# Optimization experiments

Measured on AMD Instinct MI355X. Metric: run time of the kernel, lower is better.

The kernel has to match this reference:

```python
import jax, jax.numpy as jnp
import numpy as np

NUM_EMBEDDINGS = 4096
EMBEDDING_DIM = 256
COMMITMENT_COST = 0.25


def setup_inputs() -> dict:
    key = jax.random.key(0)
    k1, k2 = jax.random.split(key)
    x = jax.random.normal(k1, (64, 32, 32, EMBEDDING_DIM), dtype=jnp.float32)
    # torch init: uniform(-1/K, 1/K)
    codebook = jax.random.uniform(
        k2, (NUM_EMBEDDINGS, EMBEDDING_DIM), dtype=jnp.float32,
        minval=-1.0 / NUM_EMBEDDINGS, maxval=1.0 / NUM_EMBEDDINGS)
    return {"x": x, "codebook": codebook}


def reference(x, codebook):
    D = codebook.shape[1]
    flat_x = x.reshape(-1, D)                                   # [N, D]
    distances = (jnp.sum(flat_x ** 2, axis=1, keepdims=True)
                 + jnp.sum(codebook ** 2, axis=1)
                 - 2.0 * flat_x @ codebook.T)                   # [N, K]
    encoding_indices = jnp.argmin(distances, axis=1)            # [N]
    quantized = codebook[encoding_indices].reshape(x.shape)     # gather (== one-hot matmul)
    q_sg = jax.lax.stop_gradient(quantized)
    x_sg = jax.lax.stop_gradient(x)
    commitment_loss = jnp.mean((q_sg - x) ** 2)
    codebook_loss = jnp.mean((quantized - x_sg) ** 2)
    vq_loss = codebook_loss + COMMITMENT_COST * commitment_loss
    # straight-through estimator
    quantized_st = x + jax.lax.stop_gradient(quantized - x)
    return quantized_st, vq_loss
```

## Files before the change

kernel.cpp:

```cpp
#include <hip/hip_runtime.h>
#include <stdint.h>

#define DIM     256
#define NCODES  4096
#define NROWS   65536
#define ROWS_WG 128
#define CCOLS   64
#define NCH     (NCODES / CCOLS)
#define CHB     (CCOLS * DIM)

#define OFF_BIMG  0u
#define OFF_HC    (1u << 20)

typedef __attribute__((ext_vector_type(8)))  int   i32x8;
typedef __attribute__((ext_vector_type(16))) float f32x16;

__device__ __forceinline__ uint32_t pk4(float a, float b, float c, float d) {
  uint32_t lo = (uint32_t)__builtin_amdgcn_cvt_pk_fp8_f32(a, b, 0, false) & 0xFFFFu;
  uint32_t hi = (uint32_t)__builtin_amdgcn_cvt_pk_fp8_f32(c, d, 0, false) & 0xFFFFu;
  return lo | (hi << 16);
}

__global__ __launch_bounds__(256) void k1_prep(const float* __restrict__ cb,
                                               uint8_t* __restrict__ ws,
                                               float* __restrict__ out,
                                               int out_size) {
  const int t = threadIdx.x;
  if (blockIdx.x == 0 && t == 0) out[out_size - 1] = 0.0f;
  const int code = blockIdx.x * 4 + (t >> 6);
  const int l = t & 63;
  float4 v = ((const float4*)(cb + (size_t)code * DIM))[l];
  float ax = v.x * 4096.0f, ay = v.y * 4096.0f;
  float az = v.z * 4096.0f, aw = v.w * 4096.0f;
  uint32_t off = (uint32_t)(code >> 6) * (uint32_t)CHB
               + (uint32_t)(l >> 2) * 1024u
               + (uint32_t)(code & 63) * 16u + (uint32_t)(l & 3) * 4u;
  *(uint32_t*)(ws + OFF_BIMG + off) = pk4(ax, ay, az, aw);
  float s = ax * ax + ay * ay + az * az + aw * aw;
  #pragma unroll
  for (int m = 1; m < 64; m <<= 1) s += __shfl_xor(s, m, 64);
  if (l == 0) ((float*)(ws + OFF_HC))[code] = 512.0f + s * (1.0f / 8192.0f);
}

__global__ __launch_bounds__(256, 2) void k2_argmin(const float* __restrict__ x,
                                                    const float* __restrict__ cb,
                                                    uint8_t* __restrict__ ws,
                                                    float* __restrict__ out,
                                                    int out_size) {
  __shared__ uint4 smem4[2048];
  char* smem = (char*)&smem4[0];
  const int t = threadIdx.x;
  const int wave = t >> 6;
  const int lane = t & 63;
  const int c = lane & 31;
  const int g = lane >> 5;
  const int wg = blockIdx.x;
  const uint8_t* __restrict__ Bimg = ws + OFF_BIMG;
  const float* __restrict__ hcg = (const float*)(ws + OFF_HC);

  const int rbw = (wave >> 1) * 64;
  const int cbw = (wave & 1) * 32;

  const float* xb = x + (size_t)wg * ROWS_WG * DIM;
  {
    #pragma unroll
    for (int it = 0; it < 16; ++it) {
      int u = it * 256 + t;
      int row = u >> 5;
      int k8 = u & 31;
      const float4* src = (const float4*)(xb + (size_t)row * DIM + k8 * 8);
      float4 v0 = src[0], v1 = src[1];
      uint32_t* d = (uint32_t*)(smem + (k8 >> 2) * 4096 + row * 32 + (k8 & 3) * 8);
      d[0] = pk4(-v0.x, -v0.y, -v0.z, -v0.w);
      d[1] = pk4(-v1.x, -v1.y, -v1.z, -v1.w);
    }
  }
  __syncthreads();

  i32x8 a[2][4];
  #pragma unroll
  for (int rt = 0; rt < 2; ++rt)
    #pragma unroll
    for (int ks = 0; ks < 4; ++ks)
      a[rt][ks] = *(const i32x8*)(smem + (ks * 2 + g) * 4096
                                  + (rbw + rt * 32 + c) * 32);

  uint32_t key[2][16];
  #pragma unroll
  for (int rt = 0; rt < 2; ++rt)
    #pragma unroll
    for (int r = 0; r < 16; ++r) key[rt][r] = 0xFFFFFFFFu;

  const int hoff = cbw + c;
  const uint32_t maskhi = 0xFFFFF000u;

  const uint8_t* gbase = Bimg + (size_t)g * 2048 + (size_t)(cbw + c) * 16;

  auto loadB = [&](uint4* dst, int ch) {
    const uint8_t* gb = gbase + (size_t)ch * CHB;
    #pragma unroll
    for (int ks = 0; ks < 4; ++ks) {
      dst[ks * 2]     = *(const uint4*)(gb + ks * 4096);
      dst[ks * 2 + 1] = *(const uint4*)(gb + ks * 4096 + 1024);
    }
  };

  auto computeC = [&](const uint4* bq, int ch, float h) {
    f32x16 acc0, acc1;
    #pragma unroll
    for (int j = 0; j < 16; ++j) { acc0[j] = h; acc1[j] = h; }
    #pragma unroll
    for (int ks = 0; ks < 4; ++ks) {
      i32x8 b;
      b[0] = (int)bq[ks * 2].x;     b[1] = (int)bq[ks * 2].y;
      b[2] = (int)bq[ks * 2].z;     b[3] = (int)bq[ks * 2].w;
      b[4] = (int)bq[ks * 2 + 1].x; b[5] = (int)bq[ks * 2 + 1].y;
      b[6] = (int)bq[ks * 2 + 1].z; b[7] = (int)bq[ks * 2 + 1].w;
      acc0 = __builtin_amdgcn_mfma_scale_f32_32x32x64_f8f6f4(
                 a[0][ks], b, acc0, 0, 0, 0, 0x7F7F7F7F, 0, 0x7F7F7F7F);
      acc1 = __builtin_amdgcn_mfma_scale_f32_32x32x64_f8f6f4(
                 a[1][ks], b, acc1, 0, 0, 0, 0x7F7F7F7F, 0, 0x7F7F7F7F);
    }
    const uint32_t col = (uint32_t)(ch * CCOLS + hoff);
    #pragma unroll
    for (int r = 0; r < 16; ++r) {
      key[0][r] = min(key[0][r], (__float_as_uint(acc0[r]) & maskhi) | col);
      key[1][r] = min(key[1][r], (__float_as_uint(acc1[r]) & maskhi) | col);
    }
  };

  uint4 bA[8], bB[8];
  float hA, hB;
  loadB(bA, 0);
  hA = hcg[hoff];
  for (int i = 0; i < NCH; i += 2) {
    loadB(bB, (i + 1) & 63);
    hB = hcg[((i + 1) & 63) * CCOLS + hoff];
    computeC(bA, i, hA);
    loadB(bA, (i + 2) & 63);
    hA = hcg[((i + 2) & 63) * CCOLS + hoff];
    computeC(bB, i + 1, hB);
  }

  #pragma unroll
  for (int rt = 0; rt < 2; ++rt)
    #pragma unroll
    for (int r = 0; r < 16; ++r) {
      uint32_t k = key[rt][r];
      #pragma unroll
      for (int m = 1; m < 32; m <<= 1) {
        uint32_t ko = (uint32_t)__shfl_xor((int)k, m, 32);
        k = min(k, ko);
      }
      key[rt][r] = k;
    }

  uint32_t* bk = (uint32_t*)smem;
  __syncthreads();
  if (t < 128) bk[t] = 0xFFFFFFFFu;
  __syncthreads();
  if (c == 0) {
    #pragma unroll
    for (int rt = 0; rt < 2; ++rt)
      #pragma unroll
      for (int r = 0; r < 16; ++r) {
        int rl = rbw + rt * 32 + (r & 3) + ((r >> 2) << 3) + (g << 2);
        atomicMin(&bk[rl], key[rt][r]);
      }
  }
  __syncthreads();

  float* ob = out + (size_t)wg * ROWS_WG * DIM;
  float psum = 0.0f;
  #pragma unroll 4
  for (int it = 0; it < 32; ++it) {
    int u = it * 256 + t;
    int row = u >> 6;
    int k4i = u & 63;
    int code = (int)(bk[row] & 0xFFFu);
    float4 q = ((const float4*)(cb + (size_t)code * DIM))[k4i];
    float4 xv = ((const float4*)xb)[u];
    ((float4*)ob)[u] = q;
    float dx = q.x - xv.x, dy = q.y - xv.y;
    float dz = q.z - xv.z, dw = q.w - xv.w;
    psum += dx * dx + dy * dy + dz * dz + dw * dw;
  }
  #pragma unroll
  for (int m = 1; m < 64; m <<= 1) psum += __shfl_xor(psum, m, 64);
  __shared__ float ps[4];
  if (lane == 0) ps[wave] = psum;
  __syncthreads();
  if (t == 0)
    atomicAdd(&out[out_size - 1],
              (ps[0] + ps[1] + ps[2] + ps[3]) * (1.25f / 16777216.0f));
}

extern "C" void kernel_launch(void* const* d_in, const int* in_sizes, int n_in,
                              void* d_out, int out_size, void* d_ws, size_t ws_size,
                              hipStream_t stream) {
  const float* x = (const float*)d_in[0];
  const float* cb = (const float*)d_in[1];
  uint8_t* ws = (uint8_t*)d_ws;
  float* out = (float*)d_out;

  k1_prep<<<dim3(NCODES / 4), dim3(256), 0, stream>>>(cb, ws, out, out_size);
  k2_argmin<<<dim3(NROWS / ROWS_WG), dim3(256), 0, stream>>>(x, cb, ws, out, out_size);
}
```

Measured before the change: 189.6 us.

## Stage codebook chunks via global_load_lds double buffering with staggered chunk order

Replaces the register double-buffered global loads of codebook fp8 chunks with direct global-to-LDS async loads into per-wave double buffers, then reads the chunk back from LDS. Each workgroup also starts at a different chunk offset so concurrent workgroups hit different parts of the codebook at the same time. This aims to free VGPRs and overlap the memory traffic with the MFMA work, but it doubles LDS use to 64KB per block. There is also no explicit wait or barrier between the async LDS writes and the reads in the next iteration, which risks a race.

After: 179.1 us. -5.5%, faster.

```diff
diff --git a/kernel.cpp b/kernel.cpp
--- a/kernel.cpp
+++ b/kernel.cpp
@@ -14,6 +14,8 @@
 
 typedef __attribute__((ext_vector_type(8)))  int   i32x8;
 typedef __attribute__((ext_vector_type(16))) float f32x16;
+typedef const __attribute__((address_space(1))) uint32_t* gas1_t;
+typedef __attribute__((address_space(3))) uint32_t*       las3_t;
 
 __device__ __forceinline__ uint32_t pk4(float a, float b, float c, float d) {
   uint32_t lo = (uint32_t)__builtin_amdgcn_cvt_pk_fp8_f32(a, b, 0, false) & 0xFFFFu;
@@ -47,7 +49,7 @@
                                                     uint8_t* __restrict__ ws,
                                                     float* __restrict__ out,
                                                     int out_size) {
-  __shared__ uint4 smem4[2048];
+  __shared__ uint4 smem4[4096];
   char* smem = (char*)&smem4[0];
   const int t = threadIdx.x;
   const int wave = t >> 6;
@@ -84,6 +86,19 @@
     for (int ks = 0; ks < 4; ++ks)
       a[rt][ks] = *(const i32x8*)(smem + (ks * 2 + g) * 4096
                                   + (rbw + rt * 32 + c) * 32);
+  __syncthreads();
+
+  char* wbuf = smem + wave * 16384;
+  auto stageW = [&](int buf, int ch) {
+    const uint8_t* gs = Bimg + (size_t)ch * CHB + (size_t)g * 1024
+                      + (size_t)(cbw + c) * 16;
+    char* lb = wbuf + buf * 8192;
+    #pragma unroll
+    for (int p = 0; p < 8; ++p)
+      __builtin_amdgcn_global_load_lds((gas1_t)(uintptr_t)(gs + p * 2048),
+                                       (las3_t)(uintptr_t)(lb + p * 1024),
+                                       16, 0, 0);
+  };
 
   uint32_t key[2][16];
   #pragma unroll
@@ -94,21 +109,30 @@
   const int hoff = cbw + c;
   const uint32_t maskhi = 0xFFFFF000u;
 
-  const uint8_t* gbase = Bimg + (size_t)g * 2048 + (size_t)(cbw + c) * 16;
-
-  auto loadB = [&](uint4* dst, int ch) {
-    const uint8_t* gb = gbase + (size_t)ch * CHB;
+  const int ch0 = ((wg * 7) + ((wg >> 8) * 29)) & 63;
+
+  stageW(0, ch0);
+  float h_cur = hcg[ch0 * CCOLS + hoff];
+
+  for (int i = 0; i < NCH; ++i) {
+    const int cur = i & 1;
+    const int ch = (ch0 + i) & 63;
+    const int chn = (ch0 + i + 1) & 63;
+
+    const char* rb = wbuf + cur * 8192 + c * 16;
+    uint4 bq[8];
     #pragma unroll
     for (int ks = 0; ks < 4; ++ks) {
-      dst[ks * 2]     = *(const uint4*)(gb + ks * 4096);
-      dst[ks * 2 + 1] = *(const uint4*)(gb + ks * 4096 + 1024);
-    }
-  };
-
-  auto computeC = [&](const uint4* bq, int ch, float h) {
+      bq[ks * 2]     = *(const uint4*)(rb + (ks * 2 + g) * 1024);
+      bq[ks * 2 + 1] = *(const uint4*)(rb + (ks * 2 + g) * 1024 + 512);
+    }
+
+    if (i + 1 < NCH) stageW(cur ^ 1, chn);
+    float h_nxt = hcg[chn * CCOLS + hoff];
+
     f32x16 acc0, acc1;
     #pragma unroll
-    for (int j = 0; j < 16; ++j) { acc0[j] = h; acc1[j] = h; }
+    for (int j = 0; j < 16; ++j) { acc0[j] = h_cur; acc1[j] = h_cur; }
     #pragma unroll
     for (int ks = 0; ks < 4; ++ks) {
       i32x8 b;
@@ -127,19 +151,7 @@
       key[0][r] = min(key[0][r], (__float_as_uint(acc0[r]) & maskhi) | col);
       key[1][r] = min(key[1][r], (__float_as_uint(acc1[r]) & maskhi) | col);
     }
-  };
-
-  uint4 bA[8], bB[8];
-  float hA, hB;
-  loadB(bA, 0);
-  hA = hcg[hoff];
-  for (int i = 0; i < NCH; i += 2) {
-    loadB(bB, (i + 1) & 63);
-    hB = hcg[((i + 1) & 63) * CCOLS + hoff];
-    computeC(bA, i, hA);
-    loadB(bA, (i + 2) & 63);
-    hA = hcg[((i + 2) & 63) * CCOLS + hoff];
-    computeC(bB, i + 1, hB);
+    h_cur = h_nxt;
   }
 
   #pragma unroll
```
